# Optimization experiments

Measured on AMD Instinct MI355X. Metric: run time of the kernel, lower is better.

The kernel has to match this reference:

```python
import jax, jax.numpy as jnp
import numpy as np

BIN_SIZE = 500   # bin_size
K = 5            # num_neighbors
D_DIM = 128      # distance_dim
MAX_BINS = 200   # max_num_bins


def _mlp(x, W1, b1, W2, b2):
    # point_wise_feed_forward_network: Dense(dff=128, elu) -> Dense(d_model)
    return jax.nn.elu(x @ W1 + b1) @ W2 + b2


def setup_inputs() -> dict:
    key = jax.random.key(0)
    ks = jax.random.split(key, 10)
    B, N, F = 8, 10000, 16
    s = 0.05
    return {
        "inputs": jax.random.normal(ks[0], (B, N, F), dtype=jnp.float32),
        # encoding MLP: F -> 128 (elu) -> D_DIM
        "W_enc1": jax.random.normal(ks[1], (F, 128), dtype=jnp.float32) * s,
        "b_enc1": jnp.zeros((128,), dtype=jnp.float32),
        "W_enc2": jax.random.normal(ks[2], (128, D_DIM), dtype=jnp.float32) * s,
        "b_enc2": jnp.zeros((D_DIM,), dtype=jnp.float32),
        # edge MLP: (2F+1) -> 128 (elu) -> 1
        "W_edge1": jax.random.normal(ks[3], (2 * F + 1, 128), dtype=jnp.float32) * s,
        "b_edge1": jnp.zeros((128,), dtype=jnp.float32),
        "W_edge2": jax.random.normal(ks[4], (128, 1), dtype=jnp.float32) * s,
        "b_edge2": jnp.zeros((1,), dtype=jnp.float32),
        # LSH codebook random rotations (non-trainable): [D_DIM, MAX_BINS//2]
        "R": jax.random.normal(ks[5], (D_DIM, MAX_BINS // 2), dtype=jnp.float32) * s,
    }


def reference(inputs, W_enc1, b_enc1, W_enc2, b_enc2,
              W_edge1, b_edge1, W_edge2, b_edge2, R):
    B, N, F = inputs.shape
    nbins = N // BIN_SIZE
    # point embeddings [B, N, D_DIM]
    enc = _mlp(inputs, W_enc1, b_enc1, W_enc2, b_enc2)

    def per_batch(x_raw, pts):
        # LSH binning: project onto random rotations, split by argmax sign bucket
        mul = pts @ R[:, :nbins // 2]                       # [N, nbins//2]
        cmul = jnp.concatenate([mul, -mul], axis=-1)        # [N, nbins]
        bin_idx = jnp.argmax(cmul, axis=-1)                 # [N]
        bins_split = jnp.argsort(bin_idx).reshape(nbins, BIN_SIZE)  # [nbins, bs]
        parts = pts[bins_split]                             # [nbins, bs, D]
        # per-bin pairwise sigmoid distance
        dm = jax.nn.sigmoid(jnp.einsum('bnd,bmd->bnm', parts, parts))
        vals, idx = jax.lax.top_k(dm, K)                    # [nbins, bs, K]
        # map bin-local neighbor indices back to global point indices
        dst = bins_split[jnp.arange(nbins)[:, None, None], idx]     # [nbins, bs, K]
        src = jnp.broadcast_to(bins_split[:, :, None], dst.shape)
        # TF stacks per-neighbor then flattens: neighbor-major order (K, nbins*bs)
        src_f = jnp.transpose(src, (2, 0, 1)).reshape(-1)
        dst_f = jnp.transpose(dst, (2, 0, 1)).reshape(-1)
        val_f = jnp.transpose(vals, (2, 0, 1)).reshape(-1)
        # tf.sparse.reorder: sort indices row-major by (src, dst)
        order = jnp.argsort(src_f * N + dst_f)
        src_s, dst_s, val_s = src_f[order], dst_f[order], val_f[order]
        # sparse edge MLP on [x_src, x_dst, dist]
        edge_in = jnp.concatenate(
            [x_raw[src_s], x_raw[dst_s], val_s[:, None]], axis=-1)  # [E, 2F+1]
        edge = jax.nn.sigmoid(
            _mlp(edge_in, W_edge1, b_edge1, W_edge2, b_edge2))[:, 0]  # [E]
        return edge, src_s, dst_s

    edge_vals, src_idx, dst_idx = jax.vmap(per_batch)(inputs, enc)
    # sparse [B, N, N]: values edge_vals[b,e] at (b, src_idx[b,e], dst_idx[b,e])
    return edge_vals, src_idx, dst_idx
```

## Files before the change

kernel.cpp:

```cpp
#include <hip/hip_runtime.h>
#include <cmath>

#define NPTS 10000
#define NBATCH 8
#define NFEAT 16
#define DDIM 128
#define NBINS 20
#define BINSZ 500
#define KSEL 5
#define EDGES_PER_BATCH (NPTS*KSEL)
#define EDGE_TOT (NBATCH*EDGES_PER_BATCH)
#define TOTPTS (NBATCH*NPTS)
#define NGRP (NBATCH*NBINS)
#define PROWS 512

typedef _Float16 f16x8 __attribute__((ext_vector_type(8)));
typedef float f32x4 __attribute__((ext_vector_type(4)));
typedef unsigned short u16;
typedef unsigned int u32;

static __device__ __forceinline__ void split_f16(float v, u16& hu, u16& du) {
    _Float16 h = (_Float16)v;
    float hf = (float)h;
    if (fabsf(v) < 6.103515625e-05f) { h = (_Float16)0.0f; hf = 0.0f; }
    _Float16 Hs = h * (_Float16)64.0f;
    _Float16 D  = (_Float16)((v - hf) * 64.0f);
    hu = __builtin_bit_cast(u16, Hs);
    du = __builtin_bit_cast(u16, D);
}

static __device__ __forceinline__ float f16bits(u16 u) {
    return (float)__builtin_bit_cast(_Float16, u);
}

__global__ __launch_bounds__(256) void k_enc(const float* __restrict__ X,
        const float* __restrict__ W1, const float* __restrict__ b1,
        const float* __restrict__ W2, const float* __restrict__ b2,
        u16* __restrict__ P, int* __restrict__ hist) {
    __shared__ float hT[128*36];
    const int tid = threadIdx.x;
    const int P0 = blockIdx.x * 32;
    if (blockIdx.x == 0 && tid < NBATCH*NBINS) hist[tid] = 0;
    #pragma unroll
    for (int i = 0; i < 16; ++i) {
        int idx = i*256 + tid;
        int p = idx >> 7;
        int j = idx & 127;
        const float* xr = X + (size_t)(P0 + p)*NFEAT;
        float h = b1[j];
        #pragma unroll
        for (int f = 0; f < 16; ++f) h += xr[f] * W1[f*128 + j];
        h = (h > 0.f) ? h : expm1f(h);
        hT[j*36 + p] = h;
    }
    __syncthreads();
    const int jt = tid & 31, pt = tid >> 5;
    const int j0 = jt*4, p0 = pt*4;
    float acc[4][4];
    #pragma unroll
    for (int ep = 0; ep < 4; ++ep)
        #pragma unroll
        for (int ej = 0; ej < 4; ++ej) acc[ep][ej] = b2[j0+ej];
    for (int k = 0; k < 128; ++k) {
        float4 hv = *(const float4*)&hT[k*36 + p0];
        float4 wv = *(const float4*)&W2[k*128 + j0];
        float hvv[4] = {hv.x,hv.y,hv.z,hv.w};
        float wvv[4] = {wv.x,wv.y,wv.z,wv.w};
        #pragma unroll
        for (int ep = 0; ep < 4; ++ep)
            #pragma unroll
            for (int ej = 0; ej < 4; ++ej) acc[ep][ej] += hvv[ep]*wvv[ej];
    }
    #pragma unroll
    for (int ep = 0; ep < 4; ++ep) {
        u16 hs[4], ds[4];
        #pragma unroll
        for (int ej = 0; ej < 4; ++ej) split_f16(acc[ep][ej], hs[ej], ds[ej]);
        size_t ro = (size_t)(P0+p0+ep)*256 + j0;
        uint2 hv2, dv2;
        hv2.x = (u32)hs[0] | ((u32)hs[1]<<16); hv2.y = (u32)hs[2] | ((u32)hs[3]<<16);
        dv2.x = (u32)ds[0] | ((u32)ds[1]<<16); dv2.y = (u32)ds[2] | ((u32)ds[3]<<16);
        *(uint2*)&P[ro]       = hv2;
        *(uint2*)&P[ro + 128] = dv2;
    }
}

__global__ __launch_bounds__(256) void k_bins(const u16* __restrict__ P,
        const float* __restrict__ R,
        int* __restrict__ binIdx, int* __restrict__ hist) {
    __shared__ float Rl[128*10];
    const int tid = threadIdx.x;
    for (int idx = tid; idx < 1280; idx += 256) {
        int d = idx / 10, i = idx % 10;
        Rl[idx] = R[d*100 + i];
    }
    __syncthreads();
    int gp = blockIdx.x*256 + tid;
    if (gp >= TOTPTS) return;
    float acc[10];
    #pragma unroll
    for (int i = 0; i < 10; ++i) acc[i] = 0.f;
    const uint4* hr = (const uint4*)(P + (size_t)gp*256);
    const uint4* lr = (const uint4*)(P + (size_t)gp*256 + 128);
    for (int c = 0; c < 16; ++c) {
        uint4 hv = hr[c], lv = lr[c];
        float x[8];
        x[0] = f16bits((u16)(hv.x & 0xffff)) + f16bits((u16)(lv.x & 0xffff));
        x[1] = f16bits((u16)(hv.x >> 16))    + f16bits((u16)(lv.x >> 16));
        x[2] = f16bits((u16)(hv.y & 0xffff)) + f16bits((u16)(lv.y & 0xffff));
        x[3] = f16bits((u16)(hv.y >> 16))    + f16bits((u16)(lv.y >> 16));
        x[4] = f16bits((u16)(hv.z & 0xffff)) + f16bits((u16)(lv.z & 0xffff));
        x[5] = f16bits((u16)(hv.z >> 16))    + f16bits((u16)(lv.z >> 16));
        x[6] = f16bits((u16)(hv.w & 0xffff)) + f16bits((u16)(lv.w & 0xffff));
        x[7] = f16bits((u16)(hv.w >> 16))    + f16bits((u16)(lv.w >> 16));
        #pragma unroll
        for (int e = 0; e < 8; ++e) {
            const float* rr = &Rl[(c*8+e)*10];
            #pragma unroll
            for (int i = 0; i < 10; ++i) acc[i] += x[e]*rr[i];
        }
    }
    float best = acc[0]; int bi = 0;
    #pragma unroll
    for (int i = 1; i < 10; ++i) if (acc[i] > best) { best = acc[i]; bi = i; }
    #pragma unroll
    for (int i = 0; i < 10; ++i) { float v = -acc[i]; if (v > best) { best = v; bi = 10+i; } }
    binIdx[gp] = bi;
    atomicAdd(&hist[(gp/NPTS)*NBINS + bi], 1);
}

__global__ __launch_bounds__(256) void k_sort(const int* __restrict__ binIdx,
        const int* __restrict__ hist, int* __restrict__ sortedIdx) {
    const int b = blockIdx.x / NBINS;
    const int bin = blockIdx.x % NBINS;
    const int tid = threadIdx.x;
    __shared__ int wtot[4];
    int off = 0;
    for (int k = 0; k < bin; ++k) off += hist[b*NBINS + k];
    const int* bptr = binIdx + b*NPTS;
    int* sptr = sortedIdx + b*NPTS;
    const int lane = tid & 63, wid = tid >> 6;
    for (int c = 0; c < 40; ++c) {
        int i = c*256 + tid;
        bool pred = (i < NPTS) && (bptr[i] == bin);
        unsigned long long mask = __ballot(pred);
        int rank = __popcll(mask & ((1ULL << lane) - 1ULL));
        if (lane == 0) wtot[wid] = __popcll(mask);
        __syncthreads();
        int prefix = 0;
        #pragma unroll
        for (int w = 0; w < 4; ++w) prefix += (w < wid) ? wtot[w] : 0;
        int total = wtot[0]+wtot[1]+wtot[2]+wtot[3];
        if (pred) sptr[off + prefix + rank] = i;
        off += total;
        __syncthreads();
    }
}

#define INS_STRICT(VV,PP,v,p) do { \
  if ((v) > VV[4]) { \
    if ((v) > VV[3]) { VV[4]=VV[3]; PP[4]=PP[3]; \
      if ((v) > VV[2]) { VV[3]=VV[2]; PP[3]=PP[2]; \
        if ((v) > VV[1]) { VV[2]=VV[1]; PP[2]=PP[1]; \
          if ((v) > VV[0]) { VV[1]=VV[0]; PP[1]=PP[0]; VV[0]=(v); PP[0]=(p); } \
          else { VV[1]=(v); PP[1]=(p); } } \
        else { VV[2]=(v); PP[2]=(p); } } \
      else { VV[3]=(v); PP[3]=(p); } } \
    else { VV[4]=(v); PP[4]=(p); } } } while(0)

#define BT(va,pa,vb,pb) (((va) > (vb)) || (((va) == (vb)) && ((pa) < (pb))))
#define INS_TIE(VV,PP,v,p) do { \
  if (BT(v,p,VV[4],PP[4])) { \
    if (BT(v,p,VV[3],PP[3])) { VV[4]=VV[3]; PP[4]=PP[3]; \
      if (BT(v,p,VV[2],PP[2])) { VV[3]=VV[2]; PP[3]=PP[2]; \
        if (BT(v,p,VV[1],PP[1])) { VV[2]=VV[1]; PP[2]=PP[1]; \
          if (BT(v,p,VV[0],PP[0])) { VV[1]=VV[0]; PP[1]=PP[0]; VV[0]=(v); PP[0]=(p); } \
          else { VV[1]=(v); PP[1]=(p); } } \
        else { VV[2]=(v); PP[2]=(p); } } \
      else { VV[3]=(v); PP[3]=(p); } } \
    else { VV[4]=(v); PP[4]=(p); } } } while(0)

__global__ __launch_bounds__(256, 4) void k_gram(const u16* __restrict__ P,
        const int* __restrict__ sortedIdx, float* __restrict__ pV, int* __restrict__ pP) {
    __shared__ int gIdx[512];
    __shared__ __align__(16) union ShU {
        struct { u16 H[128][40]; u16 L[128][40]; } bs;
        float T[64][132];
    } sh;
    const int tid = threadIdx.x;
    const int unit = blockIdx.x / 160;
    const int grp  = blockIdx.x - unit*160;
    const int rowTile = unit >> 2, ch = unit & 3;
    const int b = grp / NBINS, g = grp - b*NBINS;
    for (int i = tid; i < 512; i += 256) gIdx[i] = sortedIdx[b*NPTS + g*500 + min(i, 499)];
    __syncthreads();

    const int w    = tid >> 6;
    const int lane = tid & 63;
    const int l15  = lane & 15, l4 = lane >> 4;
    const int rowBase = rowTile * 128;

    const size_t ebase = (size_t)b * NPTS * 256;
    const u16* PB = P + ebase;
    const u16* pA0 = PB + (size_t)gIdx[rowBase + w*32 +      l15]*256 + l4*8;
    const u16* pA1 = PB + (size_t)gIdx[rowBase + w*32 + 16 + l15]*256 + l4*8;

    const int scol = tid >> 1, spart = tid & 1;
    const u16* pS = PB + (size_t)gIdx[ch*128 + scol]*256 + spart*128;
    u16* dS = spart ? &sh.bs.L[scol][0] : &sh.bs.H[scol][0];

    f32x4 acc[2][8];
    const f32x4 z4 = {0.f, 0.f, 0.f, 0.f};
    #pragma unroll
    for (int rf = 0; rf < 2; ++rf)
        #pragma unroll
        for (int cf = 0; cf < 8; ++cf) acc[rf][cf] = z4;

    uint4 s0, s1, s2, s3;
    { const uint4* s = (const uint4*)pS; s0 = s[0]; s1 = s[1]; s2 = s[2]; s3 = s[3]; }

    #pragma unroll
    for (int ks = 0; ks < 4; ++ks) {
        __syncthreads();
        {
            uint4* d = (uint4*)dS;
            d[0] = s0; d[1] = s1; d[2] = s2; d[3] = s3;
        }
        if (ks < 3) {
            const uint4* s = (const uint4*)(pS + (ks+1)*32);
            s0 = s[0]; s1 = s[1]; s2 = s[2]; s3 = s[3];
        }
        const int oH = ks*32, oD = 128 + ks*32;
        const f16x8 aH0 = *(const f16x8*)(pA0 + oH);
        const f16x8 aD0 = *(const f16x8*)(pA0 + oD);
        const f16x8 aH1 = *(const f16x8*)(pA1 + oH);
        const f16x8 aD1 = *(const f16x8*)(pA1 + oD);
        __syncthreads();
        #pragma unroll
        for (int cf = 0; cf < 8; ++cf) {
            const int col = cf*16 + l15;
            const f16x8 bH = *(const f16x8*)&sh.bs.H[col][l4*8];
            const f16x8 bD = *(const f16x8*)&sh.bs.L[col][l4*8];
            acc[0][cf] = __builtin_amdgcn_mfma_f32_16x16x32_f16(aH0, bD, acc[0][cf], 0, 0, 0);
            acc[1][cf] = __builtin_amdgcn_mfma_f32_16x16x32_f16(aH1, bD, acc[1][cf], 0, 0, 0);
            acc[0][cf] = __builtin_amdgcn_mfma_f32_16x16x32_f16(aD0, bH, acc[0][cf], 0, 0, 0);
            acc[1][cf] = __builtin_amdgcn_mfma_f32_16x16x32_f16(aD1, bH, acc[1][cf], 0, 0, 0);
            acc[0][cf] = __builtin_amdgcn_mfma_f32_16x16x32_f16(aH0, bH, acc[0][cf], 0, 0, 0);
            acc[1][cf] = __builtin_amdgcn_mfma_f32_16x16x32_f16(aH1, bH, acc[1][cf], 0, 0, 0);
        }
    }
    __syncthreads();

    const float sc = 2.44140625e-4f;
    const int rT = tid >> 2;
    const int q  = tid & 3;
    const bool chk = (ch == 3);
    #pragma unroll
    for (int rf = 0; rf < 2; ++rf) {
        #pragma unroll
        for (int cf = 0; cf < 8; ++cf) {
            const int col = cf*16 + l15;
            const int r0  = w*16 + l4*4;
            #pragma unroll
            for (int j = 0; j < 4; ++j) sh.T[r0+j][col] = acc[rf][cf][j];
        }
        __syncthreads();
        float lv[5]; int lp[5];
        #pragma unroll
        for (int p5 = 0; p5 < 5; ++p5) { lv[p5] = -3.4e38f; lp[p5] = 0x7fffffff; }
        const float* Tr = &sh.T[rT][0];
        #pragma unroll
        for (int t = 0; t < 8; ++t) {
            const int c4 = t*4 + q;
            float4 v4 = *(const float4*)&Tr[c4*4];
            float vv4[4] = {v4.x, v4.y, v4.z, v4.w};
            #pragma unroll
            for (int e = 0; e < 4; ++e) {
                const int cloc = c4*4 + e;
                if (!chk || cloc < 116)
                    INS_STRICT(lv, lp, vv4[e], ch*128 + cloc);
            }
        }
        #pragma unroll
        for (int m = 1; m < 4; m <<= 1) {
            float qv[5]; int qp[5];
            #pragma unroll
            for (int p5 = 0; p5 < 5; ++p5) {
                qv[p5] = __shfl_xor(lv[p5], m, 64);
                qp[p5] = __shfl_xor(lp[p5], m, 64);
            }
            #pragma unroll
            for (int p5 = 0; p5 < 5; ++p5) INS_TIE(lv, lp, qv[p5], qp[p5]);
        }
        if (q == 0) {
            const int rpos = rowBase + (rT>>4)*32 + rf*16 + (rT&15);
            if (rpos < 500) {
                const int pbase = ((grp*4 + ch)*PROWS + rpos)*5;
                #pragma unroll
                for (int p5 = 0; p5 < 5; ++p5) { pV[pbase+p5] = lv[p5]*sc; pP[pbase+p5] = lp[p5]; }
            }
        }
        __syncthreads();
    }
}

__global__ __launch_bounds__(256) void k_edge(const float* __restrict__ X,
        const float* __restrict__ W1, const float* __restrict__ b1,
        const float* __restrict__ W2, const float* __restrict__ b2,
        const float* __restrict__ pV, const int* __restrict__ pP,
        const int* __restrict__ sortedIdx, float* __restrict__ out) {
    __shared__ float w1t[128*36];
    __shared__ float b1l[128];
    __shared__ float w2l[128];
    const int tid = threadIdx.x;
    for (int idx = tid; idx < 33*128; idx += 256) {
        int f = idx >> 7, j = idx & 127;
        w1t[j*36 + f] = W1[idx];
    }
    if (tid < 128) { b1l[tid] = b1[tid]; w2l[tid] = W2[tid]; }
    __syncthreads();
    int rid4 = blockIdx.x*256 + tid;
    if (rid4 >= NGRP*BINSZ*4) return;
    const int rid = rid4 >> 2, quarter = rid4 & 3;
    const int grp = rid / BINSZ;
    const int rowLocal = rid - grp*BINSZ;
    const int b = grp / NBINS, g = grp - b*NBINS;
    float lv[5]; int lp[5];
    {
        int pbase = (grp*4*PROWS + rowLocal)*5;
        #pragma unroll
        for (int j = 0; j < 5; ++j) { lv[j] = pV[pbase+j]; lp[j] = pP[pbase+j]; }
    }
    #pragma unroll
    for (int chh = 1; chh < 4; ++chh) {
        int pbase = ((grp*4 + chh)*PROWS + rowLocal)*5;
        #pragma unroll
        for (int j = 0; j < 5; ++j) {
            float v = pV[pbase+j]; int p = pP[pbase+j];
            INS_TIE(lv, lp, v, p);
        }
    }
    const int* sIdx = sortedIdx + b*NPTS + g*BINSZ;
    const int src = sIdx[rowLocal];
    int dd[5]; float vv[5];
    #pragma unroll
    for (int j = 0; j < 5; ++j) {
        dd[j] = sIdx[lp[j]];
        vv[j] = 1.f/(1.f + expf(-lv[j]));
    }
    #define CSWAP(i,j) { if (dd[i] > dd[j]) { int td=dd[i];dd[i]=dd[j];dd[j]=td; \
                         float tf=vv[i];vv[i]=vv[j];vv[j]=tf; } }
    CSWAP(0,1) CSWAP(3,4) CSWAP(2,4) CSWAP(2,3) CSWAP(1,4)
    CSWAP(0,3) CSWAP(0,2) CSWAP(1,3) CSWAP(1,2)
    #undef CSWAP
    const int base = b*EDGES_PER_BATCH + src*5;
    if (quarter == 0) {
        #pragma unroll
        for (int e = 0; e < 5; ++e) {
            out[EDGE_TOT   + base + e] = (float)src;
            out[2*EDGE_TOT + base + e] = (float)dd[e];
        }
    }
    float4 xs[4];
    {
        const float4* xp = (const float4*)(X + ((size_t)b*NPTS + src)*NFEAT);
        #pragma unroll
        for (int q = 0; q < 4; ++q) xs[q] = xp[q];
    }
    float4 xd[5][4];
    #pragma unroll
    for (int e = 0; e < 5; ++e) {
        const float4* xp = (const float4*)(X + ((size_t)b*NPTS + dd[e])*NFEAT);
        #pragma unroll
        for (int q = 0; q < 4; ++q) xd[e][q] = xp[q];
    }
    float acc[5] = {0.f,0.f,0.f,0.f,0.f};
    const int jEnd = quarter*32 + 32;
    for (int j = quarter*32; j < jEnd; ++j) {
        const float* wr = &w1t[j*36];
        float4 ws0 = ((const float4*)wr)[0];
        float4 ws1 = ((const float4*)wr)[1];
        float4 ws2 = ((const float4*)wr)[2];
        float4 ws3 = ((const float4*)wr)[3];
        float4 u0  = ((const float4*)(wr+16))[0];
        float4 u1  = ((const float4*)(wr+16))[1];
        float4 u2  = ((const float4*)(wr+16))[2];
        float4 u3  = ((const float4*)(wr+16))[3];
        float w32 = wr[32];
        float w2j = w2l[j];
        float sh = b1l[j]
            + xs[0].x*ws0.x + xs[0].y*ws0.y + xs[0].z*ws0.z + xs[0].w*ws0.w
            + xs[1].x*ws1.x + xs[1].y*ws1.y + xs[1].z*ws1.z + xs[1].w*ws1.w
            + xs[2].x*ws2.x + xs[2].y*ws2.y + xs[2].z*ws2.z + xs[2].w*ws2.w
            + xs[3].x*ws3.x + xs[3].y*ws3.y + xs[3].z*ws3.z + xs[3].w*ws3.w;
        #pragma unroll
        for (int e = 0; e < 5; ++e) {
            float h = sh
                + xd[e][0].x*u0.x + xd[e][0].y*u0.y + xd[e][0].z*u0.z + xd[e][0].w*u0.w
                + xd[e][1].x*u1.x + xd[e][1].y*u1.y + xd[e][1].z*u1.z + xd[e][1].w*u1.w
                + xd[e][2].x*u2.x + xd[e][2].y*u2.y + xd[e][2].z*u2.z + xd[e][2].w*u2.w
                + xd[e][3].x*u3.x + xd[e][3].y*u3.y + xd[e][3].z*u3.z + xd[e][3].w*u3.w;
            h += vv[e]*w32;
            h = (h > 0.f) ? h : expm1f(h);
            acc[e] += h * w2j;
        }
    }
    #pragma unroll
    for (int e = 0; e < 5; ++e) {
        acc[e] += __shfl_xor(acc[e], 1, 64);
        acc[e] += __shfl_xor(acc[e], 2, 64);
    }
    if (quarter != 0) return;
    float b2v = b2[0];
    #pragma unroll
    for (int e = 0; e < 5; ++e) {
        out[base + e] = 1.f/(1.f + expf(-(acc[e] + b2v)));
    }
}

extern "C" void kernel_launch(void* const* d_in, const int* in_sizes, int n_in,
                              void* d_out, int out_size, void* d_ws, size_t ws_size,
                              hipStream_t stream) {
    const float* X   = (const float*)d_in[0];
    const float* We1 = (const float*)d_in[1];
    const float* be1 = (const float*)d_in[2];
    const float* We2 = (const float*)d_in[3];
    const float* be2 = (const float*)d_in[4];
    const float* Wd1 = (const float*)d_in[5];
    const float* bd1 = (const float*)d_in[6];
    const float* Wd2 = (const float*)d_in[7];
    const float* bd2 = (const float*)d_in[8];
    const float* R   = (const float*)d_in[9];
    float* out = (float*)d_out;

    u16* Pw         = (u16*)d_ws;
    int*   binIdx   = (int*)(Pw + (size_t)TOTPTS*256);
    int*   sortedIdx= binIdx + TOTPTS;
    int*   hist     = sortedIdx + TOTPTS;
    float* pV       = (float*)(hist + NBATCH*NBINS);
    int*   pP       = (int*)(pV + (size_t)NGRP*4*PROWS*5);

    k_enc  <<<TOTPTS/32, 256, 0, stream>>>(X, We1, be1, We2, be2, Pw, hist);
    k_bins <<<(TOTPTS+255)/256, 256, 0, stream>>>(Pw, R, binIdx, hist);
    k_sort <<<NBATCH*NBINS, 256, 0, stream>>>(binIdx, hist, sortedIdx);
    k_gram <<<NGRP*16, 256, 0, stream>>>(Pw, sortedIdx, pV, pP);
    k_edge <<<(NGRP*BINSZ*4+255)/256, 256, 0, stream>>>(X, Wd1, bd1, Wd2, bd2,
                                                        pV, pP, sortedIdx, out);
}
```

Measured before the change: 416.1 us.

## Split bin projection across four lanes per point and interleave edge weights in LDS

k_bins now assigns four threads to each point. Each thread reduces a quarter of the 128-dim embedding, and the partial sums are combined with wave shuffles, which gives four times as many threads and shorter per-thread loops for this kernel. In k_edge, the hidden units are interleaved across the four quarter-lanes, and b1 and W2 are packed into the padded W1 rows, so that adjacent lanes read distinct LDS rows and the separate arrays go away. This reduces LDS broadcast conflicts and extra loads, but adds shuffle overhead and idle lanes after the reduction in k_bins.

```diff
diff --git a/kernel.cpp b/kernel.cpp
--- a/kernel.cpp
+++ b/kernel.cpp
@@ -88,21 +88,23 @@
 __global__ __launch_bounds__(256) void k_bins(const u16* __restrict__ P,
         const float* __restrict__ R,
         int* __restrict__ binIdx, int* __restrict__ hist) {
-    __shared__ float Rl[128*10];
+    __shared__ float Rl[1280];
     const int tid = threadIdx.x;
     for (int idx = tid; idx < 1280; idx += 256) {
-        int d = idx / 10, i = idx % 10;
-        Rl[idx] = R[d*100 + i];
+        int d = idx / 10, i = idx - d*10;
+        int row = (d & 31)*4 + (d >> 5);
+        Rl[row*10 + i] = R[d*100 + i];
     }
     __syncthreads();
-    int gp = blockIdx.x*256 + tid;
-    if (gp >= TOTPTS) return;
+    const int gp4 = blockIdx.x*256 + tid;
+    const int point = gp4 >> 2, seg = gp4 & 3;
     float acc[10];
     #pragma unroll
     for (int i = 0; i < 10; ++i) acc[i] = 0.f;
-    const uint4* hr = (const uint4*)(P + (size_t)gp*256);
-    const uint4* lr = (const uint4*)(P + (size_t)gp*256 + 128);
-    for (int c = 0; c < 16; ++c) {
+    const uint4* hr = (const uint4*)(P + (size_t)point*256 + seg*32);
+    const uint4* lr = (const uint4*)(P + (size_t)point*256 + 128 + seg*32);
+    #pragma unroll
+    for (int c = 0; c < 4; ++c) {
         uint4 hv = hr[c], lv = lr[c];
         float x[8];
         x[0] = f16bits((u16)(hv.x & 0xffff)) + f16bits((u16)(lv.x & 0xffff));
@@ -115,18 +117,24 @@
         x[7] = f16bits((u16)(hv.w >> 16))    + f16bits((u16)(lv.w >> 16));
         #pragma unroll
         for (int e = 0; e < 8; ++e) {
-            const float* rr = &Rl[(c*8+e)*10];
+            const float* rr = &Rl[((c*8 + e)*4 + seg)*10];
             #pragma unroll
             for (int i = 0; i < 10; ++i) acc[i] += x[e]*rr[i];
         }
     }
+    #pragma unroll
+    for (int i = 0; i < 10; ++i) {
+        acc[i] += __shfl_xor(acc[i], 1, 64);
+        acc[i] += __shfl_xor(acc[i], 2, 64);
+    }
+    if (seg != 0) return;
     float best = acc[0]; int bi = 0;
     #pragma unroll
     for (int i = 1; i < 10; ++i) if (acc[i] > best) { best = acc[i]; bi = i; }
     #pragma unroll
     for (int i = 0; i < 10; ++i) { float v = -acc[i]; if (v > best) { best = v; bi = 10+i; } }
-    binIdx[gp] = bi;
-    atomicAdd(&hist[(gp/NPTS)*NBINS + bi], 1);
+    binIdx[point] = bi;
+    atomicAdd(&hist[(point/NPTS)*NBINS + bi], 1);
 }
 
 __global__ __launch_bounds__(256) void k_sort(const int* __restrict__ binIdx,
@@ -310,14 +318,16 @@
         const float* __restrict__ pV, const int* __restrict__ pP,
         const int* __restrict__ sortedIdx, float* __restrict__ out) {
     __shared__ float w1t[128*36];
-    __shared__ float b1l[128];
-    __shared__ float w2l[128];
     const int tid = threadIdx.x;
     for (int idx = tid; idx < 33*128; idx += 256) {
         int f = idx >> 7, j = idx & 127;
-        w1t[j*36 + f] = W1[idx];
-    }
-    if (tid < 128) { b1l[tid] = b1[tid]; w2l[tid] = W2[tid]; }
+        w1t[((j & 31)*4 + (j >> 5))*36 + f] = W1[idx];
+    }
+    if (tid < 128) {
+        int r = ((tid & 31)*4 + (tid >> 5))*36;
+        w1t[r + 33] = b1[tid];
+        w1t[r + 34] = W2[tid];
+    }
     __syncthreads();
     int rid4 = blockIdx.x*256 + tid;
     if (rid4 >= NGRP*BINSZ*4) return;
@@ -375,9 +385,8 @@
         for (int q = 0; q < 4; ++q) xd[e][q] = xp[q];
     }
     float acc[5] = {0.f,0.f,0.f,0.f,0.f};
-    const int jEnd = quarter*32 + 32;
-    for (int j = quarter*32; j < jEnd; ++j) {
-        const float* wr = &w1t[j*36];
+    for (int jj = 0; jj < 32; ++jj) {
+        const float* wr = &w1t[(jj*4 + quarter)*36];
         float4 ws0 = ((const float4*)wr)[0];
         float4 ws1 = ((const float4*)wr)[1];
         float4 ws2 = ((const float4*)wr)[2];
@@ -387,8 +396,9 @@
         float4 u2  = ((const float4*)(wr+16))[2];
         float4 u3  = ((const float4*)(wr+16))[3];
         float w32 = wr[32];
-        float w2j = w2l[j];
-        float sh = b1l[j]
+        float b1j = wr[33];
+        float w2j = wr[34];
+        float sh = b1j
             + xs[0].x*ws0.x + xs[0].y*ws0.y + xs[0].z*ws0.z + xs[0].w*ws0.w
             + xs[1].x*ws1.x + xs[1].y*ws1.y + xs[1].z*ws1.z + xs[1].w*ws1.w
             + xs[2].x*ws2.x + xs[2].y*ws2.y + xs[2].z*ws2.z + xs[2].w*ws2.w
@@ -441,7 +451,7 @@
     int*   pP       = (int*)(pV + (size_t)NGRP*4*PROWS*5);
 
     k_enc  <<<TOTPTS/32, 256, 0, stream>>>(X, We1, be1, We2, be2, Pw, hist);
-    k_bins <<<(TOTPTS+255)/256, 256, 0, stream>>>(Pw, R, binIdx, hist);
+    k_bins <<<TOTPTS*4/256, 256, 0, stream>>>(Pw, R, binIdx, hist);
     k_sort <<<NBATCH*NBINS, 256, 0, stream>>>(binIdx, hist, sortedIdx);
     k_gram <<<NGRP*16, 256, 0, stream>>>(Pw, sortedIdx, pV, pP);
     k_edge <<<(NGRP*BINSZ*4+255)/256, 256, 0, stream>>>(X, Wd1, bd1, Wd2, bd2,
```

After: 403.6 us. -3.0%, faster.
